# Performance work log

Measured on AMD Instinct MI355X. Metric: run time of the kernel, lower is better.

Reference implementation:

```python
import jax, jax.numpy as jnp
import numpy as np

B, SQ, SK, D = 8, 512, 512, 32


def _spd_cov(key, b, s, d):
    # random SPD covariance: A A^T + I
    a = 0.1 * jax.random.normal(key, (b, s, d, d), dtype=jnp.float32)
    return jnp.einsum('bsde,bsfe->bsdf', a, a) + jnp.eye(d, dtype=jnp.float32)


def setup_inputs() -> dict:
    key = jax.random.key(0)
    ks = jax.random.split(key, 6)
    return {
        'q_mean': jax.random.normal(ks[0], (B, SQ, D), dtype=jnp.float32),
        'q_cov': _spd_cov(ks[1], B, SQ, D),
        'k_mean': jax.random.normal(ks[2], (B, SK, D), dtype=jnp.float32),
        'k_cov': _spd_cov(ks[3], B, SK, D),
        'v_mean': jax.random.normal(ks[4], (B, SK, D), dtype=jnp.float32),
        'v_cov': _spd_cov(ks[5], B, SK, D),
    }


def reference(q_mean, q_cov, k_mean, k_cov, v_mean, v_cov):
    # Pairwise symmetric Gaussian JSD attention.
    # JSD = 0.5*(KL(p_q||p_k)+KL(p_k||p_q)); the log-det terms cancel:
    # JSD = 0.25*( tr(Sk^-1 Sq) + tr(Sq^-1 Sk) - 2D
    #              + dm^T (Sk^-1 + Sq^-1) dm ),  dm = mu_q - mu_k
    d = q_mean.shape[-1]
    q_inv = jnp.linalg.inv(q_cov)            # [B,Sq,D,D]
    k_inv = jnp.linalg.inv(k_cov)            # [B,Sk,D,D]
    tr_kq = jnp.einsum('bkde,bqed->bqk', k_inv, q_cov)
    tr_qk = jnp.einsum('bqde,bked->bqk', q_inv, k_cov)
    dm = q_mean[:, :, None, :] - k_mean[:, None, :, :]   # [B,Sq,Sk,D]
    quad = (jnp.einsum('bqkd,bkde,bqke->bqk', dm, k_inv, dm)
            + jnp.einsum('bqkd,bqde,bqke->bqk', dm, q_inv, dm))
    js = 0.25 * (tr_kq + tr_qk - 2.0 * d + quad)         # [B,Sq,Sk]
    score = jax.nn.softmax(js, axis=-1)
    out_mean = jnp.einsum('bqk,bkd->bqd', score, v_mean)
    out_cov = jnp.einsum('bqk,bkde->bqde', score, v_cov)
    return out_mean, out_cov
```

## Files before the change

### kernel.cpp

```cpp
#include <hip/hip_runtime.h>
#include <hip/hip_bf16.h>

#define NBATCH 8
#define SQL 512
#define SKL 512
#define DD 32
#define KF 1152
#define UT 528
#define NOUT 1056
#define NVT 1088
#define NSITE (NBATCH * SQL)
#define VS_BLOCKS (34 * 16 * NBATCH)

typedef short short8 __attribute__((ext_vector_type(8)));
typedef float f32x4 __attribute__((ext_vector_type(4)));
typedef unsigned short ushort_t;

__device__ __forceinline__ ushort_t f2bf(float f) {
    unsigned int u = __float_as_uint(f);
    return (ushort_t)((u + 0x7fffu + ((u >> 16) & 1u)) >> 16);
}
__device__ __forceinline__ float bf2f(ushort_t h) {
    return __uint_as_float(((unsigned int)h) << 16);
}
__device__ __forceinline__ void gl_lds16(const ushort_t* g, ushort_t* l) {
    __builtin_amdgcn_global_load_lds(
        (const __attribute__((address_space(1))) void*)g,
        (__attribute__((address_space(3))) void*)l, 16, 0, 0);
}
__device__ __forceinline__ void pk_split(float v0, float v1, ushort_t& h0, ushort_t& h1,
                                         ushort_t& l0, ushort_t& l1) {
    __hip_bfloat162 H = __float22bfloat162_rn(make_float2(v0, v1));
    ushort2 hu = *(ushort2*)&H;
    h0 = hu.x; h1 = hu.y;
    __hip_bfloat162 L = __float22bfloat162_rn(make_float2(v0 - bf2f(hu.x), v1 - bf2f(hu.y)));
    ushort2 lu = *(ushort2*)&L;
    l0 = lu.x; l1 = lu.y;
}

template<int P>
__device__ __forceinline__ float swzb(float x) {
    return __int_as_float(__builtin_amdgcn_ds_swizzle(__float_as_int(x), (P << 5)));
}
template<int M>
__device__ __forceinline__ float swzx(float x) {
    return __int_as_float(__builtin_amdgcn_ds_swizzle(__float_as_int(x), (M << 10) | 0x1F));
}

template<int P>
__device__ __forceinline__ void gj_step(float (&a)[DD], int hl) {
    float piv = swzb<P>(a[P]);
    float rinv = __builtin_amdgcn_rcpf(piv);
    float t = a[P] * rinv;
    bool isp = (hl == P);
    float u = isp ? rinv : t;
    float g = isp ? 0.0f : 1.0f;
    #pragma unroll
    for (int i = 0; i < DD; ++i) {
        if (i == P) continue;
        float ci = swzb<P>(a[i]);
        a[i] = fmaf(a[i], g, -(ci * u));
    }
    a[P] = u;
}
template<int P>
__device__ __forceinline__ void gj_run(float (&a)[DD], int hl) {
    gj_step<P>(a, hl);
    if constexpr (P + 1 < DD) gj_run<P + 1>(a, hl);
}

__global__ __launch_bounds__(256, 8) void feat_kernel(
    const float* __restrict__ qm, const float* __restrict__ qc,
    const float* __restrict__ km, const float* __restrict__ kc,
    ushort_t* __restrict__ fqh, ushort_t* __restrict__ fql,
    ushort_t* __restrict__ fkh, ushort_t* __restrict__ fkl)
{
    __shared__ float smem[8 * 560];

    const int tid = threadIdx.x;
    const int wid = tid >> 6, lane = tid & 63;
    const int half = lane >> 5, hl = lane & 31;
    const int site_g = (blockIdx.x * 4 + wid) * 2 + half;
    const int qside = site_g < NSITE;
    const int site = qside ? site_g : site_g - NSITE;

    const float* covp = (qside ? qc : kc) + (size_t)site * (DD * DD);
    const float* mup  = (qside ? qm : km) + (size_t)site * DD;
    ushort_t* fh = qside ? fqh : fkh;
    ushort_t* fl = qside ? fql : fkl;
    const size_t fo = (size_t)site * KF;

    float* inv_p = smem + (wid * 2 + half) * 560;
    float* mu_s  = inv_p + 528;

    const float mu_lane = mup[hl];
    mu_s[hl] = mu_lane;

    float a[DD];
    #pragma unroll
    for (int r = 0; r < DD; ++r) a[r] = covp[r * DD + hl];

    gj_run<0>(a, hl);

    #pragma unroll
    for (int r = 0; r < DD; ++r)
        if (r <= hl) inv_p[((r * (65 - r)) >> 1) + hl - r] = a[r];

    float ivr = 0.f;
    #pragma unroll
    for (int e = 0; e < DD; ++e) ivr = fmaf(a[e], mu_s[e], ivr);

    float pb = mu_lane * ivr;
    pb += swzx<1>(pb); pb += swzx<2>(pb); pb += swzx<4>(pb);
    pb += swzx<8>(pb); pb += swzx<16>(pb);
    const float bias = pb;

    for (int idx = hl; idx < UT; idx += 32) {
        int d = (int)((65.0f - sqrtf(4225.0f - 8.0f * (float)idx)) * 0.5f);
        if (d > 0 && (d * (65 - d)) / 2 > idx) --d;
        if (((d + 1) * (64 - d)) / 2 <= idx) ++d;
        int off = (d * (65 - d)) / 2;
        int e = d + (idx - off);
        float Mv = covp[d * DD + e] + mu_s[d] * mu_s[e];
        float Iv = inv_p[idx];
        float w = (d == e) ? 0.25f : 0.5f;
        float v0, v1;
        if (qside) { v0 = w * Mv; v1 = w * Iv; }
        else       { v0 = Iv;     v1 = Mv; }
        ushort_t h0, h1, l0, l1;
        pk_split(v0, v1, h0, h1, l0, l1);
        fh[fo + idx] = h0; fh[fo + UT + idx] = h1;
        fl[fo + idx] = l0; fl[fo + UT + idx] = l1;
    }
    {
        float v0, v1;
        if (qside) { v0 = -0.5f * ivr; v1 = 0.25f * mu_lane; }
        else       { v0 = mu_lane;     v1 = -2.f * ivr; }
        ushort_t h0, h1, l0, l1;
        pk_split(v0, v1, h0, h1, l0, l1);
        fh[fo + 2*UT + hl] = h0; fh[fo + 2*UT + DD + hl] = h1;
        fl[fo + 2*UT + hl] = l0; fl[fo + 2*UT + DD + hl] = l1;
    }
    if (hl == 0) {
        float v = qside ? 0.25f : bias;
        ushort_t hb = f2bf(v);
        fh[fo + 2*UT + 2*DD] = hb;
        fl[fo + 2*UT + 2*DD] = f2bf(v - bf2f(hb));
    }
    for (int i = 2*UT + 2*DD + 1 + hl; i < KF; i += 32) { fh[fo + i] = 0; fl[fo + i] = 0; }
}

template<int MODE, int DUAL>
__global__ __launch_bounds__(256) void gemm_split(
    const ushort_t* __restrict__ Ah_g, const ushort_t* __restrict__ Al_g,
    const ushort_t* __restrict__ Bh_g, const ushort_t* __restrict__ Bl_g,
    float* __restrict__ C0, float* __restrict__ C1)
{
    constexpr bool SPLIT = (MODE == 0);
    constexpr int KSTRIDE = SPLIT ? KF : SKL;
    constexpr int KITERS = SPLIT ? (KF / 2 / 32) : (SKL / 32);
    const int b = blockIdx.z, nt = blockIdx.x;
    const int mt = SPLIT ? (blockIdx.y & 3) : blockIdx.y;
    const int ks = SPLIT ? (blockIdx.y >> 2) : 0;
    const int kbase = ks * (SPLIT ? (KF / 2) : 0);
    const int tid = threadIdx.x, lane = tid & 63, wid = tid >> 6;
    const int wm = wid & 1, wn = wid >> 1;
    const int BROWS = MODE ? NVT : SKL;

    const ushort_t* Ah = Ah_g + ((size_t)b * SQL + mt * 128) * KSTRIDE;
    const ushort_t* Al = Al_g + ((size_t)b * SQL + mt * 128) * KSTRIDE;
    const ushort_t* Bh = Bh_g + ((size_t)b * BROWS + nt * 64) * KSTRIDE;
    const ushort_t* Bl = Bl_g + ((size_t)b * BROWS + nt * 64) * KSTRIDE;

    __shared__ __align__(16) ushort_t AsH[128 * 32];
    __shared__ __align__(16) ushort_t AsL[SPLIT ? 128 * 32 : 8];
    __shared__ __align__(16) ushort_t BsH[64 * 32];
    __shared__ __align__(16) ushort_t BsL[SPLIT ? 64 * 32 : 8];

    const int r4 = lane >> 2, kp = (lane & 3) * 8;
    const int arow0 = wid * 16 + r4,        aoff0 = wid * 512 + lane * 8;
    const int arow1 = (wid + 4) * 16 + r4,  aoff1 = (wid + 4) * 512 + lane * 8;

    const int fm = lane & 15;
    const int q8 = (lane >> 4) * 8;

    f32x4 acc[4][2];
    #pragma unroll
    for (int i = 0; i < 4; ++i)
        #pragma unroll
        for (int j = 0; j < 2; ++j)
            acc[i][j] = (f32x4){0.f, 0.f, 0.f, 0.f};

    for (int it = 0; it < KITERS; ++it) {
        const int k0 = kbase + it * 32;
        __syncthreads();
        gl_lds16(Ah + (size_t)arow0 * KSTRIDE + k0 + kp, &AsH[aoff0]);
        gl_lds16(Ah + (size_t)arow1 * KSTRIDE + k0 + kp, &AsH[aoff1]);
        gl_lds16(Bh + (size_t)arow0 * KSTRIDE + k0 + kp, &BsH[aoff0]);
        if (SPLIT) {
            gl_lds16(Al + (size_t)arow0 * KSTRIDE + k0 + kp, &AsL[aoff0]);
            gl_lds16(Al + (size_t)arow1 * KSTRIDE + k0 + kp, &AsL[aoff1]);
            gl_lds16(Bl + (size_t)arow0 * KSTRIDE + k0 + kp, &BsL[aoff0]);
        }
        __syncthreads();

        short8 ah[4], al[4], bh[2], bl[2];
        #pragma unroll
        for (int i = 0; i < 4; ++i) {
            const int r = wm * 64 + i * 16 + fm;
            ah[i] = *(const short8*)&AsH[r * 32 + q8];
            if (SPLIT) al[i] = *(const short8*)&AsL[r * 32 + q8];
        }
        #pragma unroll
        for (int j = 0; j < 2; ++j) {
            const int r = wn * 32 + j * 16 + fm;
            bh[j] = *(const short8*)&BsH[r * 32 + q8];
            if (SPLIT) bl[j] = *(const short8*)&BsL[r * 32 + q8];
        }
        #pragma unroll
        for (int i = 0; i < 4; ++i)
            #pragma unroll
            for (int j = 0; j < 2; ++j) {
                acc[i][j] = __builtin_amdgcn_mfma_f32_16x16x32_bf16(ah[i], bh[j], acc[i][j], 0, 0, 0);
                if (SPLIT) {
                    acc[i][j] = __builtin_amdgcn_mfma_f32_16x16x32_bf16(ah[i], bl[j], acc[i][j], 0, 0, 0);
                    acc[i][j] = __builtin_amdgcn_mfma_f32_16x16x32_bf16(al[i], bh[j], acc[i][j], 0, 0, 0);
                }
            }
    }

    float* Cs = (SPLIT && DUAL && ks) ? C1 : C0;
    const int crow0 = (lane >> 4) * 4;
    const int ccol = lane & 15;
    #pragma unroll
    for (int i = 0; i < 4; ++i) {
        const int m = mt * 128 + wm * 64 + i * 16 + crow0;
        #pragma unroll
        for (int j = 0; j < 2; ++j) {
            const int n = nt * 64 + wn * 32 + j * 16 + ccol;
            #pragma unroll
            for (int r = 0; r < 4; ++r) {
                const float v = acc[i][j][r];
                const size_t rowb = (size_t)b * SQL + (m + r);
                if (MODE == 0) {
                    if (DUAL) Cs[rowb * SKL + n] = v;
                    else      atomicAdd(&C0[rowb * SKL + n], v);
                } else {
                    if (n < DD)        C0[rowb * DD + n] = v;
                    else if (n < NOUT) C1[rowb * (DD * DD) + (n - DD)] = v;
                }
            }
        }
    }
}

template<int DUAL>
__global__ __launch_bounds__(256) void phase2_kernel(
    const float* __restrict__ js0, const float* __restrict__ js1,
    ushort_t* __restrict__ ph,
    const float* __restrict__ vmean, const float* __restrict__ vcov,
    ushort_t* __restrict__ vth)
{
    __shared__ float sm[32 * 33];
    const int tid = threadIdx.x;
    if (blockIdx.x < (unsigned)(NBATCH * SQL)) {
        const size_t ro = (size_t)blockIdx.x * SKL + 2 * tid;
        float2 v = *(const float2*)(js0 + ro);
        if (DUAL) {
            float2 v1 = *(const float2*)(js1 + ro);
            v.x += v1.x; v.y += v1.y;
        }
        float m = fmaxf(v.x, v.y);
        #pragma unroll
        for (int o = 32; o > 0; o >>= 1) m = fmaxf(m, __shfl_xor(m, o));
        const int wid = tid >> 6, ln = tid & 63;
        if (ln == 0) sm[wid] = m;
        __syncthreads();
        m = fmaxf(fmaxf(sm[0], sm[1]), fmaxf(sm[2], sm[3]));
        float e0 = __expf(v.x - m), e1 = __expf(v.y - m);
        float s = e0 + e1;
        #pragma unroll
        for (int o = 32; o > 0; o >>= 1) s += __shfl_xor(s, o);
        if (ln == 0) sm[4 + wid] = s;
        __syncthreads();
        s = sm[4] + sm[5] + sm[6] + sm[7];
        float rs = 1.0f / s;
        ph[ro]     = f2bf(e0 * rs);
        ph[ro + 1] = f2bf(e1 * rs);
    } else {
        const int vb = blockIdx.x - NBATCH * SQL;
        const int b = vb / (34 * 16), rem = vb % (34 * 16);
        const int kt = rem / 34, nt = rem % 34;
        const int n0 = nt * 32, k0 = kt * 32;
        const int tx = tid & 31, ty = tid >> 5;
        for (int r = ty; r < 32; r += 8) {
            const int k = k0 + r, n = n0 + tx;
            float v;
            if (n0 == 0)          v = vmean[((size_t)b * SKL + k) * DD + n];
            else if (n0 >= NOUT)  v = 0.f;
            else                  v = vcov[((size_t)b * SKL + k) * (DD * DD) + (n - DD)];
            sm[tx * 33 + r] = v;
        }
        __syncthreads();
        for (int r = ty; r < 32; r += 8) {
            const int n = n0 + r, k = k0 + tx;
            vth[((size_t)b * NVT + n) * SKL + k] = f2bf(sm[r * 33 + tx]);
        }
    }
}

extern "C" void kernel_launch(void* const* d_in, const int* in_sizes, int n_in,
                              void* d_out, int out_size, void* d_ws, size_t ws_size,
                              hipStream_t stream)
{
    const float* q_mean = (const float*)d_in[0];
    const float* q_cov  = (const float*)d_in[1];
    const float* k_mean = (const float*)d_in[2];
    const float* k_cov  = (const float*)d_in[3];
    const float* v_mean = (const float*)d_in[4];
    const float* v_cov  = (const float*)d_in[5];

    float* out_mean = (float*)d_out;
    float* out_cov  = out_mean + (size_t)NBATCH * SQL * DD;

    char* w = (char*)d_ws;
    const size_t FQN = (size_t)NBATCH * SQL * KF;
    const size_t JSN = (size_t)NBATCH * SQL * SKL;
    ushort_t* fq_h = (ushort_t*)w;
    ushort_t* fq_l = fq_h + FQN;
    ushort_t* fk_h = fq_l + FQN;
    ushort_t* fk_l = fk_h + FQN;
    float*    js0  = (float*)(fk_l + FQN);
    float*    js1  = js0 + JSN;
    ushort_t* vt_h = fq_h;
    ushort_t* p_h  = fk_h;

    const bool dual = ws_size >= (8 * FQN + 8 * JSN);

    feat_kernel<<<2 * NSITE / 8, 256, 0, stream>>>(
        q_mean, q_cov, k_mean, k_cov, fq_h, fq_l, fk_h, fk_l);
    if (dual) {
        gemm_split<0, 1><<<dim3(SKL / 64, 8, NBATCH), 256, 0, stream>>>(
            fq_h, fq_l, fk_h, fk_l, js0, js1);
        phase2_kernel<1><<<NBATCH * SQL + VS_BLOCKS, 256, 0, stream>>>(
            js0, js1, p_h, v_mean, v_cov, vt_h);
    } else {
        hipMemsetAsync(js0, 0, JSN * sizeof(float), stream);
        gemm_split<0, 0><<<dim3(SKL / 64, 8, NBATCH), 256, 0, stream>>>(
            fq_h, fq_l, fk_h, fk_l, js0, nullptr);
        phase2_kernel<0><<<NBATCH * SQL + VS_BLOCKS, 256, 0, stream>>>(
            js0, nullptr, p_h, v_mean, v_cov, vt_h);
    }
    gemm_split<1, 0><<<dim3(NVT / 64, SQL / 128, NBATCH), 256, 0, stream>>>(
        p_h, nullptr, vt_h, nullptr, out_mean, out_cov);
}
```

Before: 191.5 us.

## Fuse V transpose into feature kernel and switch GJ pivot broadcast to LDS

The V-matrix bf16 transpose moves out of the softmax kernel into the feature kernel as extra blocks, with its own workspace region, so it no longer has to wait for the score GEMM. The Gauss-Jordan inversion now broadcasts each pivot row through LDS with float4 reads instead of one ds_swizzle per element, using a sign-flipped sweep formulation whose result is negated at the end. Launch bounds drop from 8 to 4 waves to allow more registers. The extra workspace may make the dual-buffer path less likely to be chosen, and lower occupancy could hurt latency hiding.

New measurement: 476.3 us. 2.49x slower.

```diff
diff --git a/kernel.cpp b/kernel.cpp
--- a/kernel.cpp
+++ b/kernel.cpp
@@ -10,6 +10,7 @@
 #define NOUT 1056
 #define NVT 1088
 #define NSITE (NBATCH * SQL)
+#define FEAT_BLOCKS (2 * NSITE / 8)
 #define VS_BLOCKS (34 * 16 * NBATCH)
 
 typedef short short8 __attribute__((ext_vector_type(8)));
@@ -37,117 +38,146 @@
     ushort2 lu = *(ushort2*)&L;
     l0 = lu.x; l1 = lu.y;
 }
-
-template<int P>
-__device__ __forceinline__ float swzb(float x) {
-    return __int_as_float(__builtin_amdgcn_ds_swizzle(__float_as_int(x), (P << 5)));
-}
 template<int M>
 __device__ __forceinline__ float swzx(float x) {
     return __int_as_float(__builtin_amdgcn_ds_swizzle(__float_as_int(x), (M << 10) | 0x1F));
 }
 
 template<int P>
-__device__ __forceinline__ void gj_step(float (&a)[DD], int hl) {
-    float piv = swzb<P>(a[P]);
-    float rinv = __builtin_amdgcn_rcpf(piv);
-    float t = a[P] * rinv;
-    bool isp = (hl == P);
-    float u = isp ? rinv : t;
-    float g = isp ? 0.0f : 1.0f;
+__device__ __forceinline__ void sweep_step(float (&a)[DD], int hl, float* pc) {
+    pc[hl] = a[P];
+    float c[DD];
+    #pragma unroll
+    for (int q = 0; q < 8; ++q) {
+        float4 v = ((const float4*)pc)[q];
+        c[q * 4 + 0] = v.x; c[q * 4 + 1] = v.y;
+        c[q * 4 + 2] = v.z; c[q * 4 + 3] = v.w;
+    }
+    const float d = c[P];
+    const float rinv = __builtin_amdgcn_rcpf(d);
+    const float t = a[P] * rinv;
+    const bool isp = (hl == P);
+    const float alpha = isp ? 0.0f : 1.0f;
+    const float beta  = isp ? rinv : -t;
     #pragma unroll
     for (int i = 0; i < DD; ++i) {
         if (i == P) continue;
-        float ci = swzb<P>(a[i]);
-        a[i] = fmaf(a[i], g, -(ci * u));
-    }
-    a[P] = u;
+        a[i] = fmaf(c[i], beta, a[i] * alpha);
+    }
+    a[P] = isp ? -rinv : t;
 }
 template<int P>
-__device__ __forceinline__ void gj_run(float (&a)[DD], int hl) {
-    gj_step<P>(a, hl);
-    if constexpr (P + 1 < DD) gj_run<P + 1>(a, hl);
-}
-
-__global__ __launch_bounds__(256, 8) void feat_kernel(
+__device__ __forceinline__ void sweep_run(float (&a)[DD], int hl, float* pc) {
+    sweep_step<P>(a, hl, pc);
+    if constexpr (P + 1 < DD) sweep_run<P + 1>(a, hl, pc);
+}
+
+__global__ __launch_bounds__(256, 4) void feat_fused(
     const float* __restrict__ qm, const float* __restrict__ qc,
     const float* __restrict__ km, const float* __restrict__ kc,
     ushort_t* __restrict__ fqh, ushort_t* __restrict__ fql,
-    ushort_t* __restrict__ fkh, ushort_t* __restrict__ fkl)
+    ushort_t* __restrict__ fkh, ushort_t* __restrict__ fkl,
+    const float* __restrict__ vmean, const float* __restrict__ vcov,
+    ushort_t* __restrict__ vth)
 {
-    __shared__ float smem[8 * 560];
-
+    __shared__ float smem[8 * 592];
     const int tid = threadIdx.x;
-    const int wid = tid >> 6, lane = tid & 63;
-    const int half = lane >> 5, hl = lane & 31;
-    const int site_g = (blockIdx.x * 4 + wid) * 2 + half;
-    const int qside = site_g < NSITE;
-    const int site = qside ? site_g : site_g - NSITE;
-
-    const float* covp = (qside ? qc : kc) + (size_t)site * (DD * DD);
-    const float* mup  = (qside ? qm : km) + (size_t)site * DD;
-    ushort_t* fh = qside ? fqh : fkh;
-    ushort_t* fl = qside ? fql : fkl;
-    const size_t fo = (size_t)site * KF;
-
-    float* inv_p = smem + (wid * 2 + half) * 560;
-    float* mu_s  = inv_p + 528;
-
-    const float mu_lane = mup[hl];
-    mu_s[hl] = mu_lane;
-
-    float a[DD];
-    #pragma unroll
-    for (int r = 0; r < DD; ++r) a[r] = covp[r * DD + hl];
-
-    gj_run<0>(a, hl);
-
-    #pragma unroll
-    for (int r = 0; r < DD; ++r)
-        if (r <= hl) inv_p[((r * (65 - r)) >> 1) + hl - r] = a[r];
-
-    float ivr = 0.f;
-    #pragma unroll
-    for (int e = 0; e < DD; ++e) ivr = fmaf(a[e], mu_s[e], ivr);
-
-    float pb = mu_lane * ivr;
-    pb += swzx<1>(pb); pb += swzx<2>(pb); pb += swzx<4>(pb);
-    pb += swzx<8>(pb); pb += swzx<16>(pb);
-    const float bias = pb;
-
-    for (int idx = hl; idx < UT; idx += 32) {
-        int d = (int)((65.0f - sqrtf(4225.0f - 8.0f * (float)idx)) * 0.5f);
-        if (d > 0 && (d * (65 - d)) / 2 > idx) --d;
-        if (((d + 1) * (64 - d)) / 2 <= idx) ++d;
-        int off = (d * (65 - d)) / 2;
-        int e = d + (idx - off);
-        float Mv = covp[d * DD + e] + mu_s[d] * mu_s[e];
-        float Iv = inv_p[idx];
-        float w = (d == e) ? 0.25f : 0.5f;
-        float v0, v1;
-        if (qside) { v0 = w * Mv; v1 = w * Iv; }
-        else       { v0 = Iv;     v1 = Mv; }
-        ushort_t h0, h1, l0, l1;
-        pk_split(v0, v1, h0, h1, l0, l1);
-        fh[fo + idx] = h0; fh[fo + UT + idx] = h1;
-        fl[fo + idx] = l0; fl[fo + UT + idx] = l1;
-    }
-    {
-        float v0, v1;
-        if (qside) { v0 = -0.5f * ivr; v1 = 0.25f * mu_lane; }
-        else       { v0 = mu_lane;     v1 = -2.f * ivr; }
-        ushort_t h0, h1, l0, l1;
-        pk_split(v0, v1, h0, h1, l0, l1);
-        fh[fo + 2*UT + hl] = h0; fh[fo + 2*UT + DD + hl] = h1;
-        fl[fo + 2*UT + hl] = l0; fl[fo + 2*UT + DD + hl] = l1;
-    }
-    if (hl == 0) {
-        float v = qside ? 0.25f : bias;
-        ushort_t hb = f2bf(v);
-        fh[fo + 2*UT + 2*DD] = hb;
-        fl[fo + 2*UT + 2*DD] = f2bf(v - bf2f(hb));
-    }
-    for (int i = 2*UT + 2*DD + 1 + hl; i < KF; i += 32) { fh[fo + i] = 0; fl[fo + i] = 0; }
+
+    if (blockIdx.x < FEAT_BLOCKS) {
+        const int wid = tid >> 6, lane = tid & 63;
+        const int half = lane >> 5, hl = lane & 31;
+        const int site_g = (blockIdx.x * 4 + wid) * 2 + half;
+        const int qside = site_g < NSITE;
+        const int site = qside ? site_g : site_g - NSITE;
+
+        const float* covp = (qside ? qc : kc) + (size_t)site * (DD * DD);
+        const float* mup  = (qside ? qm : km) + (size_t)site * DD;
+        ushort_t* fh = qside ? fqh : fkh;
+        ushort_t* fl = qside ? fql : fkl;
+        const size_t fo = (size_t)site * KF;
+
+        float* base  = smem + (wid * 2 + half) * 592;
+        float* inv_p = base;
+        float* mu_s  = base + 528;
+        float* pc    = base + 560;
+
+        const float mu_lane = mup[hl];
+        mu_s[hl] = mu_lane;
+
+        float a[DD];
+        #pragma unroll
+        for (int r = 0; r < DD; ++r) a[r] = covp[r * DD + hl];
+
+        sweep_run<0>(a, hl, pc);
+
+        #pragma unroll
+        for (int r = 0; r < DD; ++r)
+            if (r <= hl) inv_p[((r * (65 - r)) >> 1) + hl - r] = -a[r];
+
+        float s = 0.f;
+        #pragma unroll
+        for (int e = 0; e < DD; ++e) s = fmaf(a[e], mu_s[e], s);
+        const float ivr = -s;
+
+        float pb = mu_lane * ivr;
+        pb += swzx<1>(pb); pb += swzx<2>(pb); pb += swzx<4>(pb);
+        pb += swzx<8>(pb); pb += swzx<16>(pb);
+        const float bias = pb;
+
+        for (int idx = hl; idx < UT; idx += 32) {
+            int d = (int)((65.0f - sqrtf(4225.0f - 8.0f * (float)idx)) * 0.5f);
+            if (d > 0 && (d * (65 - d)) / 2 > idx) --d;
+            if (((d + 1) * (64 - d)) / 2 <= idx) ++d;
+            int off = (d * (65 - d)) / 2;
+            int e = d + (idx - off);
+            float Mv = covp[d * DD + e] + mu_s[d] * mu_s[e];
+            float Iv = inv_p[idx];
+            float w = (d == e) ? 0.25f : 0.5f;
+            float v0, v1;
+            if (qside) { v0 = w * Mv; v1 = w * Iv; }
+            else       { v0 = Iv;     v1 = Mv; }
+            ushort_t h0, h1, l0, l1;
+            pk_split(v0, v1, h0, h1, l0, l1);
+            fh[fo + idx] = h0; fh[fo + UT + idx] = h1;
+            fl[fo + idx] = l0; fl[fo + UT + idx] = l1;
+        }
+        {
+            float v0, v1;
+            if (qside) { v0 = -0.5f * ivr; v1 = 0.25f * mu_lane; }
+            else       { v0 = mu_lane;     v1 = -2.f * ivr; }
+            ushort_t h0, h1, l0, l1;
+            pk_split(v0, v1, h0, h1, l0, l1);
+            fh[fo + 2*UT + hl] = h0; fh[fo + 2*UT + DD + hl] = h1;
+            fl[fo + 2*UT + hl] = l0; fl[fo + 2*UT + DD + hl] = l1;
+        }
+        if (hl == 0) {
+            float v = qside ? 0.25f : bias;
+            ushort_t hb = f2bf(v);
+            fh[fo + 2*UT + 2*DD] = hb;
+            fl[fo + 2*UT + 2*DD] = f2bf(v - bf2f(hb));
+        }
+        for (int i = 2*UT + 2*DD + 1 + hl; i < KF; i += 32) { fh[fo + i] = 0; fl[fo + i] = 0; }
+    } else {
+        float* sm = smem;
+        const int vb = blockIdx.x - FEAT_BLOCKS;
+        const int b = vb / (34 * 16), rem = vb % (34 * 16);
+        const int kt = rem / 34, nt = rem % 34;
+        const int n0 = nt * 32, k0 = kt * 32;
+        const int tx = tid & 31, ty = tid >> 5;
+        for (int r = ty; r < 32; r += 8) {
+            const int k = k0 + r, n = n0 + tx;
+            float v;
+            if (n0 == 0)          v = vmean[((size_t)b * SKL + k) * DD + n];
+            else if (n0 >= NOUT)  v = 0.f;
+            else                  v = vcov[((size_t)b * SKL + k) * (DD * DD) + (n - DD)];
+            sm[tx * 33 + r] = v;
+        }
+        __syncthreads();
+        for (int r = ty; r < 32; r += 8) {
+            const int n = n0 + r, k = k0 + tx;
+            vth[((size_t)b * NVT + n) * SKL + k] = f2bf(sm[r * 33 + tx]);
+        }
+    }
 }
 
 template<int MODE, int DUAL>
@@ -255,58 +285,35 @@
 }
 
 template<int DUAL>
-__global__ __launch_bounds__(256) void phase2_kernel(
+__global__ __launch_bounds__(256) void softmax_rows(
     const float* __restrict__ js0, const float* __restrict__ js1,
-    ushort_t* __restrict__ ph,
-    const float* __restrict__ vmean, const float* __restrict__ vcov,
-    ushort_t* __restrict__ vth)
+    ushort_t* __restrict__ ph)
 {
-    __shared__ float sm[32 * 33];
+    __shared__ float sm[8];
     const int tid = threadIdx.x;
-    if (blockIdx.x < (unsigned)(NBATCH * SQL)) {
-        const size_t ro = (size_t)blockIdx.x * SKL + 2 * tid;
-        float2 v = *(const float2*)(js0 + ro);
-        if (DUAL) {
-            float2 v1 = *(const float2*)(js1 + ro);
-            v.x += v1.x; v.y += v1.y;
-        }
-        float m = fmaxf(v.x, v.y);
-        #pragma unroll
-        for (int o = 32; o > 0; o >>= 1) m = fmaxf(m, __shfl_xor(m, o));
-        const int wid = tid >> 6, ln = tid & 63;
-        if (ln == 0) sm[wid] = m;
-        __syncthreads();
-        m = fmaxf(fmaxf(sm[0], sm[1]), fmaxf(sm[2], sm[3]));
-        float e0 = __expf(v.x - m), e1 = __expf(v.y - m);
-        float s = e0 + e1;
-        #pragma unroll
-        for (int o = 32; o > 0; o >>= 1) s += __shfl_xor(s, o);
-        if (ln == 0) sm[4 + wid] = s;
-        __syncthreads();
-        s = sm[4] + sm[5] + sm[6] + sm[7];
-        float rs = 1.0f / s;
-        ph[ro]     = f2bf(e0 * rs);
-        ph[ro + 1] = f2bf(e1 * rs);
-    } else {
-        const int vb = blockIdx.x - NBATCH * SQL;
-        const int b = vb / (34 * 16), rem = vb % (34 * 16);
-        const int kt = rem / 34, nt = rem % 34;
-        const int n0 = nt * 32, k0 = kt * 32;
-        const int tx = tid & 31, ty = tid >> 5;
-        for (int r = ty; r < 32; r += 8) {
-            const int k = k0 + r, n = n0 + tx;
-            float v;
-            if (n0 == 0)          v = vmean[((size_t)b * SKL + k) * DD + n];
-            else if (n0 >= NOUT)  v = 0.f;
-            else                  v = vcov[((size_t)b * SKL + k) * (DD * DD) + (n - DD)];
-            sm[tx * 33 + r] = v;
-        }
-        __syncthreads();
-        for (int r = ty; r < 32; r += 8) {
-            const int n = n0 + r, k = k0 + tx;
-            vth[((size_t)b * NVT + n) * SKL + k] = f2bf(sm[r * 33 + tx]);
-        }
-    }
+    const size_t ro = (size_t)blockIdx.x * SKL + 2 * tid;
+    float2 v = *(const float2*)(js0 + ro);
+    if (DUAL) {
+        float2 v1 = *(const float2*)(js1 + ro);
+        v.x += v1.x; v.y += v1.y;
+    }
+    float m = fmaxf(v.x, v.y);
+    #pragma unroll
+    for (int o = 32; o > 0; o >>= 1) m = fmaxf(m, __shfl_xor(m, o));
+    const int wid = tid >> 6, ln = tid & 63;
+    if (ln == 0) sm[wid] = m;
+    __syncthreads();
+    m = fmaxf(fmaxf(sm[0], sm[1]), fmaxf(sm[2], sm[3]));
+    float e0 = __expf(v.x - m), e1 = __expf(v.y - m);
+    float s = e0 + e1;
+    #pragma unroll
+    for (int o = 32; o > 0; o >>= 1) s += __shfl_xor(s, o);
+    if (ln == 0) sm[4 + wid] = s;
+    __syncthreads();
+    s = sm[4] + sm[5] + sm[6] + sm[7];
+    float rs = 1.0f / s;
+    ph[ro]     = f2bf(e0 * rs);
+    ph[ro + 1] = f2bf(e1 * rs);
 }
 
 extern "C" void kernel_launch(void* const* d_in, const int* in_sizes, int n_in,
@@ -326,30 +333,29 @@
     char* w = (char*)d_ws;
     const size_t FQN = (size_t)NBATCH * SQL * KF;
     const size_t JSN = (size_t)NBATCH * SQL * SKL;
+    const size_t VTN = (size_t)NBATCH * NVT * SKL;
     ushort_t* fq_h = (ushort_t*)w;
     ushort_t* fq_l = fq_h + FQN;
     ushort_t* fk_h = fq_l + FQN;
     ushort_t* fk_l = fk_h + FQN;
     float*    js0  = (float*)(fk_l + FQN);
-    float*    js1  = js0 + JSN;
-    ushort_t* vt_h = fq_h;
+    const bool dual = ws_size >= (8 * FQN + 8 * JSN + 2 * VTN);
+    float*    js1  = dual ? (js0 + JSN) : nullptr;
+    ushort_t* vt_h = (ushort_t*)(js0 + (dual ? 2 : 1) * JSN);
     ushort_t* p_h  = fk_h;
 
-    const bool dual = ws_size >= (8 * FQN + 8 * JSN);
-
-    feat_kernel<<<2 * NSITE / 8, 256, 0, stream>>>(
-        q_mean, q_cov, k_mean, k_cov, fq_h, fq_l, fk_h, fk_l);
+    feat_fused<<<FEAT_BLOCKS + VS_BLOCKS, 256, 0, stream>>>(
+        q_mean, q_cov, k_mean, k_cov, fq_h, fq_l, fk_h, fk_l,
+        v_mean, v_cov, vt_h);
     if (dual) {
         gemm_split<0, 1><<<dim3(SKL / 64, 8, NBATCH), 256, 0, stream>>>(
             fq_h, fq_l, fk_h, fk_l, js0, js1);
-        phase2_kernel<1><<<NBATCH * SQL + VS_BLOCKS, 256, 0, stream>>>(
-            js0, js1, p_h, v_mean, v_cov, vt_h);
+        softmax_rows<1><<<NBATCH * SQL, 256, 0, stream>>>(js0, js1, p_h);
     } else {
         hipMemsetAsync(js0, 0, JSN * sizeof(float), stream);
         gemm_split<0, 0><<<dim3(SKL / 64, 8, NBATCH), 256, 0, stream>>>(
             fq_h, fq_l, fk_h, fk_l, js0, nullptr);
-        phase2_kernel<0><<<NBATCH * SQL + VS_BLOCKS, 256, 0, stream>>>(
-            js0, nullptr, p_h, v_mean, v_cov, vt_h);
+        softmax_rows<0><<<NBATCH * SQL, 256, 0, stream>>>(js0, nullptr, p_h);
     }
     gemm_split<1, 0><<<dim3(NVT / 64, SQL / 128, NBATCH), 256, 0, stream>>>(
         p_h, nullptr, vt_h, nullptr, out_mean, out_cov);
```

## Move V transpose into feature kernel and store inverse as padded square

Applied to the files above, without the earlier changes.

The V-mean/V-cov bf16 transpose blocks move out of the post-GEMM phase2 kernel into the first feature kernel, so they run alongside the Gauss-Jordan feature blocks and leave softmax as its own lighter kernel. Because the feature buffers are still live at that point, vt_h gets its own workspace region, and dual mode now needs more workspace. The inverse is also kept in a padded 33-stride square in LDS instead of a packed triangle. This roughly doubles the feature kernel's LDS, and its launch bounds drop from 8 to 4 blocks, which may reduce occupancy for the inversion work.

After: 184.3 us. 1.04x faster.

```diff
diff --git a/kernel.cpp b/kernel.cpp
--- a/kernel.cpp
+++ b/kernel.cpp
@@ -10,6 +10,7 @@
 #define NOUT 1056
 #define NVT 1088
 #define NSITE (NBATCH * SQL)
+#define FEAT_BLOCKS (2 * NSITE / 8)
 #define VS_BLOCKS (34 * 16 * NBATCH)
 
 typedef short short8 __attribute__((ext_vector_type(8)));
@@ -69,85 +70,108 @@
     if constexpr (P + 1 < DD) gj_run<P + 1>(a, hl);
 }
 
-__global__ __launch_bounds__(256, 8) void feat_kernel(
+__global__ __launch_bounds__(256, 4) void feat_fused(
     const float* __restrict__ qm, const float* __restrict__ qc,
     const float* __restrict__ km, const float* __restrict__ kc,
     ushort_t* __restrict__ fqh, ushort_t* __restrict__ fql,
-    ushort_t* __restrict__ fkh, ushort_t* __restrict__ fkl)
+    ushort_t* __restrict__ fkh, ushort_t* __restrict__ fkl,
+    const float* __restrict__ vmean, const float* __restrict__ vcov,
+    ushort_t* __restrict__ vth)
 {
-    __shared__ float smem[8 * 560];
-
+    __shared__ float smem[8 * 1064 + 8 * 32];
     const int tid = threadIdx.x;
-    const int wid = tid >> 6, lane = tid & 63;
-    const int half = lane >> 5, hl = lane & 31;
-    const int site_g = (blockIdx.x * 4 + wid) * 2 + half;
-    const int qside = site_g < NSITE;
-    const int site = qside ? site_g : site_g - NSITE;
-
-    const float* covp = (qside ? qc : kc) + (size_t)site * (DD * DD);
-    const float* mup  = (qside ? qm : km) + (size_t)site * DD;
-    ushort_t* fh = qside ? fqh : fkh;
-    ushort_t* fl = qside ? fql : fkl;
-    const size_t fo = (size_t)site * KF;
-
-    float* inv_p = smem + (wid * 2 + half) * 560;
-    float* mu_s  = inv_p + 528;
-
-    const float mu_lane = mup[hl];
-    mu_s[hl] = mu_lane;
-
-    float a[DD];
-    #pragma unroll
-    for (int r = 0; r < DD; ++r) a[r] = covp[r * DD + hl];
-
-    gj_run<0>(a, hl);
-
-    #pragma unroll
-    for (int r = 0; r < DD; ++r)
-        if (r <= hl) inv_p[((r * (65 - r)) >> 1) + hl - r] = a[r];
-
-    float ivr = 0.f;
-    #pragma unroll
-    for (int e = 0; e < DD; ++e) ivr = fmaf(a[e], mu_s[e], ivr);
-
-    float pb = mu_lane * ivr;
-    pb += swzx<1>(pb); pb += swzx<2>(pb); pb += swzx<4>(pb);
-    pb += swzx<8>(pb); pb += swzx<16>(pb);
-    const float bias = pb;
-
-    for (int idx = hl; idx < UT; idx += 32) {
-        int d = (int)((65.0f - sqrtf(4225.0f - 8.0f * (float)idx)) * 0.5f);
-        if (d > 0 && (d * (65 - d)) / 2 > idx) --d;
-        if (((d + 1) * (64 - d)) / 2 <= idx) ++d;
-        int off = (d * (65 - d)) / 2;
-        int e = d + (idx - off);
-        float Mv = covp[d * DD + e] + mu_s[d] * mu_s[e];
-        float Iv = inv_p[idx];
-        float w = (d == e) ? 0.25f : 0.5f;
-        float v0, v1;
-        if (qside) { v0 = w * Mv; v1 = w * Iv; }
-        else       { v0 = Iv;     v1 = Mv; }
-        ushort_t h0, h1, l0, l1;
-        pk_split(v0, v1, h0, h1, l0, l1);
-        fh[fo + idx] = h0; fh[fo + UT + idx] = h1;
-        fl[fo + idx] = l0; fl[fo + UT + idx] = l1;
-    }
-    {
-        float v0, v1;
-        if (qside) { v0 = -0.5f * ivr; v1 = 0.25f * mu_lane; }
-        else       { v0 = mu_lane;     v1 = -2.f * ivr; }
-        ushort_t h0, h1, l0, l1;
-        pk_split(v0, v1, h0, h1, l0, l1);
-        fh[fo + 2*UT + hl] = h0; fh[fo + 2*UT + DD + hl] = h1;
-        fl[fo + 2*UT + hl] = l0; fl[fo + 2*UT + DD + hl] = l1;
-    }
-    if (hl == 0) {
-        float v = qside ? 0.25f : bias;
-        ushort_t hb = f2bf(v);
-        fh[fo + 2*UT + 2*DD] = hb;
-        fl[fo + 2*UT + 2*DD] = f2bf(v - bf2f(hb));
-    }
-    for (int i = 2*UT + 2*DD + 1 + hl; i < KF; i += 32) { fh[fo + i] = 0; fl[fo + i] = 0; }
+
+    if (blockIdx.x < FEAT_BLOCKS) {
+        const int wid = tid >> 6, lane = tid & 63;
+        const int half = lane >> 5, hl = lane & 31;
+        const int site_g = (blockIdx.x * 4 + wid) * 2 + half;
+        const int qside = site_g < NSITE;
+        const int site = qside ? site_g : site_g - NSITE;
+
+        const float* covp = (qside ? qc : kc) + (size_t)site * (DD * DD);
+        const float* mup  = (qside ? qm : km) + (size_t)site * DD;
+        ushort_t* fh = qside ? fqh : fkh;
+        ushort_t* fl = qside ? fql : fkl;
+        const size_t fo = (size_t)site * KF;
+
+        float* inv_s = smem + (wid * 2 + half) * 1064;
+        float* mu_s  = smem + 8 * 1064 + (wid * 2 + half) * 32;
+
+        const float mu_lane = mup[hl];
+        mu_s[hl] = mu_lane;
+
+        float a[DD];
+        #pragma unroll
+        for (int r = 0; r < DD; ++r) a[r] = covp[r * DD + hl];
+
+        gj_run<0>(a, hl);
+
+        #pragma unroll
+        for (int r = 0; r < DD; ++r) inv_s[r * 33 + hl] = a[r];
+
+        float ivr = 0.f;
+        #pragma unroll
+        for (int e = 0; e < DD; ++e) ivr = fmaf(a[e], mu_s[e], ivr);
+
+        float pb = mu_lane * ivr;
+        pb += swzx<1>(pb); pb += swzx<2>(pb); pb += swzx<4>(pb);
+        pb += swzx<8>(pb); pb += swzx<16>(pb);
+        const float bias = pb;
+
+        for (int idx = hl; idx < UT; idx += 32) {
+            int d = (int)((65.0f - sqrtf(4225.0f - 8.0f * (float)idx)) * 0.5f);
+            if (d > 0 && (d * (65 - d)) / 2 > idx) --d;
+            if (((d + 1) * (64 - d)) / 2 <= idx) ++d;
+            int off = (d * (65 - d)) / 2;
+            int e = d + (idx - off);
+            float Mv = covp[d * DD + e] + mu_s[d] * mu_s[e];
+            float Iv = inv_s[d * 33 + e];
+            float w = (d == e) ? 0.25f : 0.5f;
+            float v0, v1;
+            if (qside) { v0 = w * Mv; v1 = w * Iv; }
+            else       { v0 = Iv;     v1 = Mv; }
+            ushort_t h0, h1, l0, l1;
+            pk_split(v0, v1, h0, h1, l0, l1);
+            fh[fo + idx] = h0; fh[fo + UT + idx] = h1;
+            fl[fo + idx] = l0; fl[fo + UT + idx] = l1;
+        }
+        {
+            float v0, v1;
+            if (qside) { v0 = -0.5f * ivr; v1 = 0.25f * mu_lane; }
+            else       { v0 = mu_lane;     v1 = -2.f * ivr; }
+            ushort_t h0, h1, l0, l1;
+            pk_split(v0, v1, h0, h1, l0, l1);
+            fh[fo + 2*UT + hl] = h0; fh[fo + 2*UT + DD + hl] = h1;
+            fl[fo + 2*UT + hl] = l0; fl[fo + 2*UT + DD + hl] = l1;
+        }
+        if (hl == 0) {
+            float v = qside ? 0.25f : bias;
+            ushort_t hb = f2bf(v);
+            fh[fo + 2*UT + 2*DD] = hb;
+            fl[fo + 2*UT + 2*DD] = f2bf(v - bf2f(hb));
+        }
+        for (int i = 2*UT + 2*DD + 1 + hl; i < KF; i += 32) { fh[fo + i] = 0; fl[fo + i] = 0; }
+    } else {
+        float* sm = smem;
+        const int vb = blockIdx.x - FEAT_BLOCKS;
+        const int b = vb / (34 * 16), rem = vb % (34 * 16);
+        const int kt = rem / 34, nt = rem % 34;
+        const int n0 = nt * 32, k0 = kt * 32;
+        const int tx = tid & 31, ty = tid >> 5;
+        for (int r = ty; r < 32; r += 8) {
+            const int k = k0 + r, n = n0 + tx;
+            float v;
+            if (n0 == 0)          v = vmean[((size_t)b * SKL + k) * DD + n];
+            else if (n0 >= NOUT)  v = 0.f;
+            else                  v = vcov[((size_t)b * SKL + k) * (DD * DD) + (n - DD)];
+            sm[tx * 33 + r] = v;
+        }
+        __syncthreads();
+        for (int r = ty; r < 32; r += 8) {
+            const int n = n0 + r, k = k0 + tx;
+            vth[((size_t)b * NVT + n) * SKL + k] = f2bf(sm[r * 33 + tx]);
+        }
+    }
 }
 
 template<int MODE, int DUAL>
@@ -255,58 +279,35 @@
 }
 
 template<int DUAL>
-__global__ __launch_bounds__(256) void phase2_kernel(
+__global__ __launch_bounds__(256) void softmax_rows(
     const float* __restrict__ js0, const float* __restrict__ js1,
-    ushort_t* __restrict__ ph,
-    const float* __restrict__ vmean, const float* __restrict__ vcov,
-    ushort_t* __restrict__ vth)
+    ushort_t* __restrict__ ph)
 {
-    __shared__ float sm[32 * 33];
+    __shared__ float sm[8];
     const int tid = threadIdx.x;
-    if (blockIdx.x < (unsigned)(NBATCH * SQL)) {
-        const size_t ro = (size_t)blockIdx.x * SKL + 2 * tid;
-        float2 v = *(const float2*)(js0 + ro);
-        if (DUAL) {
-            float2 v1 = *(const float2*)(js1 + ro);
-            v.x += v1.x; v.y += v1.y;
-        }
-        float m = fmaxf(v.x, v.y);
-        #pragma unroll
-        for (int o = 32; o > 0; o >>= 1) m = fmaxf(m, __shfl_xor(m, o));
-        const int wid = tid >> 6, ln = tid & 63;
-        if (ln == 0) sm[wid] = m;
-        __syncthreads();
-        m = fmaxf(fmaxf(sm[0], sm[1]), fmaxf(sm[2], sm[3]));
-        float e0 = __expf(v.x - m), e1 = __expf(v.y - m);
-        float s = e0 + e1;
-        #pragma unroll
-        for (int o = 32; o > 0; o >>= 1) s += __shfl_xor(s, o);
-        if (ln == 0) sm[4 + wid] = s;
-        __syncthreads();
-        s = sm[4] + sm[5] + sm[6] + sm[7];
-        float rs = 1.0f / s;
-        ph[ro]     = f2bf(e0 * rs);
-        ph[ro + 1] = f2bf(e1 * rs);
-    } else {
-        const int vb = blockIdx.x - NBATCH * SQL;
-        const int b = vb / (34 * 16), rem = vb % (34 * 16);
-        const int kt = rem / 34, nt = rem % 34;
-        const int n0 = nt * 32, k0 = kt * 32;
-        const int tx = tid & 31, ty = tid >> 5;
-        for (int r = ty; r < 32; r += 8) {
-            const int k = k0 + r, n = n0 + tx;
-            float v;
-            if (n0 == 0)          v = vmean[((size_t)b * SKL + k) * DD + n];
-            else if (n0 >= NOUT)  v = 0.f;
-            else                  v = vcov[((size_t)b * SKL + k) * (DD * DD) + (n - DD)];
-            sm[tx * 33 + r] = v;
-        }
-        __syncthreads();
-        for (int r = ty; r < 32; r += 8) {
-            const int n = n0 + r, k = k0 + tx;
-            vth[((size_t)b * NVT + n) * SKL + k] = f2bf(sm[r * 33 + tx]);
-        }
-    }
+    const size_t ro = (size_t)blockIdx.x * SKL + 2 * tid;
+    float2 v = *(const float2*)(js0 + ro);
+    if (DUAL) {
+        float2 v1 = *(const float2*)(js1 + ro);
+        v.x += v1.x; v.y += v1.y;
+    }
+    float m = fmaxf(v.x, v.y);
+    #pragma unroll
+    for (int o = 32; o > 0; o >>= 1) m = fmaxf(m, __shfl_xor(m, o));
+    const int wid = tid >> 6, ln = tid & 63;
+    if (ln == 0) sm[wid] = m;
+    __syncthreads();
+    m = fmaxf(fmaxf(sm[0], sm[1]), fmaxf(sm[2], sm[3]));
+    float e0 = __expf(v.x - m), e1 = __expf(v.y - m);
+    float s = e0 + e1;
+    #pragma unroll
+    for (int o = 32; o > 0; o >>= 1) s += __shfl_xor(s, o);
+    if (ln == 0) sm[4 + wid] = s;
+    __syncthreads();
+    s = sm[4] + sm[5] + sm[6] + sm[7];
+    float rs = 1.0f / s;
+    ph[ro]     = f2bf(e0 * rs);
+    ph[ro + 1] = f2bf(e1 * rs);
 }
 
 extern "C" void kernel_launch(void* const* d_in, const int* in_sizes, int n_in,
@@ -326,30 +327,29 @@
     char* w = (char*)d_ws;
     const size_t FQN = (size_t)NBATCH * SQL * KF;
     const size_t JSN = (size_t)NBATCH * SQL * SKL;
+    const size_t VTN = (size_t)NBATCH * NVT * SKL;
     ushort_t* fq_h = (ushort_t*)w;
     ushort_t* fq_l = fq_h + FQN;
     ushort_t* fk_h = fq_l + FQN;
     ushort_t* fk_l = fk_h + FQN;
     float*    js0  = (float*)(fk_l + FQN);
-    float*    js1  = js0 + JSN;
-    ushort_t* vt_h = fq_h;
+    const bool dual = ws_size >= (8 * FQN + 8 * JSN + 2 * VTN);
+    float*    js1  = dual ? (js0 + JSN) : nullptr;
+    ushort_t* vt_h = (ushort_t*)(js0 + (dual ? 2 : 1) * JSN);
     ushort_t* p_h  = fk_h;
 
-    const bool dual = ws_size >= (8 * FQN + 8 * JSN);
-
-    feat_kernel<<<2 * NSITE / 8, 256, 0, stream>>>(
-        q_mean, q_cov, k_mean, k_cov, fq_h, fq_l, fk_h, fk_l);
+    feat_fused<<<FEAT_BLOCKS + VS_BLOCKS, 256, 0, stream>>>(
+        q_mean, q_cov, k_mean, k_cov, fq_h, fq_l, fk_h, fk_l,
+        v_mean, v_cov, vt_h);
     if (dual) {
         gemm_split<0, 1><<<dim3(SKL / 64, 8, NBATCH), 256, 0, stream>>>(
             fq_h, fq_l, fk_h, fk_l, js0, js1);
-        phase2_kernel<1><<<NBATCH * SQL + VS_BLOCKS, 256, 0, stream>>>(
-            js0, js1, p_h, v_mean, v_cov, vt_h);
+        softmax_rows<1><<<NBATCH * SQL, 256, 0, stream>>>(js0, js1, p_h);
     } else {
         hipMemsetAsync(js0, 0, JSN * sizeof(float), stream);
         gemm_split<0, 0><<<dim3(SKL / 64, 8, NBATCH), 256, 0, stream>>>(
             fq_h, fq_l, fk_h, fk_l, js0, nullptr);
-        phase2_kernel<0><<<NBATCH * SQL + VS_BLOCKS, 256, 0, stream>>>(
-            js0, nullptr, p_h, v_mean, v_cov, vt_h);
+        softmax_rows<0><<<NBATCH * SQL, 256, 0, stream>>>(js0, nullptr, p_h);
     }
     gemm_split<1, 0><<<dim3(NVT / 64, SQL / 128, NBATCH), 256, 0, stream>>>(
         p_h, nullptr, vt_h, nullptr, out_mean, out_cov);
```
